# Performance work log

Hardware: AMD Instinct MI355X
Metric: run time of the kernel (lower is better)

The kernel has to match this reference:

```python
import jax, jax.numpy as jnp
import numpy as np

ENZ_DIM, CPD_DIM, OUT_DIM = 1280, 256, 512
B, L_ENZ, L_CPD = 32, 512, 128
SCALE = OUT_DIM ** 0.5


def _linear_params(key, d_in, d_out):
    k1, k2 = jax.random.split(key)
    lim = 1.0 / np.sqrt(d_in)
    W = jax.random.uniform(k1, (d_in, d_out), jnp.float32, -lim, lim)
    b = jax.random.uniform(k2, (d_out,), jnp.float32, -lim, lim)
    return W, b


def setup_inputs() -> dict:
    key = jax.random.key(0)
    ks = jax.random.split(key, 16)
    inp = {
        "enz_node_feature": jax.random.normal(ks[0], (B, L_ENZ, ENZ_DIM), jnp.float32),
        "substrate_node_feature": jax.random.normal(ks[1], (B, L_CPD, CPD_DIM), jnp.float32),
        "product_node_feature": jax.random.normal(ks[2], (B, L_CPD, CPD_DIM), jnp.float32),
        "enz_node_feature_mask": jnp.ones((B, L_ENZ), dtype=bool),
        "substrate_node_feature_mask": jnp.ones((B, L_CPD), dtype=bool),
        "product_node_feature_mask": jnp.ones((B, L_CPD), dtype=bool),
        "interaction_weight": jax.random.normal(ks[3], (B, L_CPD, L_ENZ), jnp.float32),
    }
    # cross_attn_enzyme: query=enz (ENZ_DIM), key/value=cpd (CPD_DIM)
    inp["enz_Wq"], inp["enz_bq"] = _linear_params(ks[4], ENZ_DIM, OUT_DIM)
    inp["enz_Wk"], inp["enz_bk"] = _linear_params(ks[5], CPD_DIM, OUT_DIM)
    inp["enz_Wv"], inp["enz_bv"] = _linear_params(ks[6], CPD_DIM, OUT_DIM)
    # cross_attn_substrate: query=cpd, key/value=enz
    inp["sub_Wq"], inp["sub_bq"] = _linear_params(ks[7], CPD_DIM, OUT_DIM)
    inp["sub_Wk"], inp["sub_bk"] = _linear_params(ks[8], ENZ_DIM, OUT_DIM)
    inp["sub_Wv"], inp["sub_bv"] = _linear_params(ks[9], ENZ_DIM, OUT_DIM)
    # cross_attn_product: query=cpd, key/value=enz
    inp["prod_Wq"], inp["prod_bq"] = _linear_params(ks[10], CPD_DIM, OUT_DIM)
    inp["prod_Wk"], inp["prod_bk"] = _linear_params(ks[11], ENZ_DIM, OUT_DIM)
    inp["prod_Wv"], inp["prod_bv"] = _linear_params(ks[12], ENZ_DIM, OUT_DIM)
    return inp


def _cross_attn(q_in, k_in, v_in, q_mask, k_mask, Wq, bq, Wk, bk, Wv, bv, attn_bias=None):
    q = q_in @ Wq + bq          # [B, Lq, D]
    k = k_in @ Wk + bk          # [B, Lk, D]
    v = v_in @ Wv + bv          # [B, Lk, D]
    scores = jnp.einsum("bqd,bkd->bqk", q, k) / SCALE
    if attn_bias is not None:
        scores = scores + attn_bias
    mask = q_mask[:, :, None] & k_mask[:, None, :]   # [B, Lq, Lk]
    scores = jnp.where(mask, scores, -1e9)
    w = jax.nn.softmax(scores, axis=-1)
    return jnp.einsum("bqk,bkd->bqd", w, v)


def reference(enz_node_feature, substrate_node_feature, product_node_feature,
              enz_node_feature_mask, substrate_node_feature_mask, product_node_feature_mask,
              interaction_weight,
              enz_Wq, enz_bq, enz_Wk, enz_bk, enz_Wv, enz_bv,
              sub_Wq, sub_bq, sub_Wk, sub_bk, sub_Wv, sub_bv,
              prod_Wq, prod_bq, prod_Wk, prod_bk, prod_Wv, prod_bv):
    subs_pocket_weight = interaction_weight                       # [B, L_cpd, L_enz]
    pocket_subs_weight = jnp.swapaxes(interaction_weight, 1, 2)   # [B, L_enz, L_cpd]

    enzyme_subs = _cross_attn(enz_node_feature, substrate_node_feature, substrate_node_feature,
                              enz_node_feature_mask, substrate_node_feature_mask,
                              enz_Wq, enz_bq, enz_Wk, enz_bk, enz_Wv, enz_bv,
                              attn_bias=pocket_subs_weight)
    subs_enzyme = _cross_attn(substrate_node_feature, enz_node_feature, enz_node_feature,
                              substrate_node_feature_mask, enz_node_feature_mask,
                              sub_Wq, sub_bq, sub_Wk, sub_bk, sub_Wv, sub_bv,
                              attn_bias=subs_pocket_weight)
    # product path reuses cross_attn_enzyme weights for enz->prod (as in torch code)
    enzyme_prod = _cross_attn(enz_node_feature, product_node_feature, product_node_feature,
                              enz_node_feature_mask, product_node_feature_mask,
                              enz_Wq, enz_bq, enz_Wk, enz_bk, enz_Wv, enz_bv)
    prod_enzyme = _cross_attn(product_node_feature, enz_node_feature, enz_node_feature,
                              product_node_feature_mask, enz_node_feature_mask,
                              prod_Wq, prod_bq, prod_Wk, prod_bk, prod_Wv, prod_bv)

    return jnp.concatenate([enzyme_subs.mean(axis=1), subs_enzyme.mean(axis=1),
                            enzyme_prod.mean(axis=1), prod_enzyme.mean(axis=1)], axis=-1)
```

## Files before the change

### kernel.cpp

```cpp
#include <hip/hip_runtime.h>
#include <cstdint>
#include <cstddef>


#define SCALE_INV 0.044194173824159216f

typedef short bf16x8 __attribute__((ext_vector_type(8)));
typedef float f32x4  __attribute__((ext_vector_type(4)));

__device__ __forceinline__ ushort f2bf(float f) {
  union { float f; unsigned u; } c; c.f = f;
  unsigned u = c.u + 0x7fffu + ((c.u >> 16) & 1u);
  return (ushort)(u >> 16);
}
__device__ __forceinline__ float bf2f(ushort h) {
  return __uint_as_float(((unsigned)h) << 16);
}
__device__ __forceinline__ void gload16(const ushort* g, ushort* l) {
  __builtin_amdgcn_global_load_lds(
      (const __attribute__((address_space(1))) void*)g,
      (__attribute__((address_space(3))) void*)l, 16, 0, 0);
}

__device__ __forceinline__ void cvt8(const float* __restrict__ in,
                                     ushort* __restrict__ out, int blk, int n) {
  int i = (blk * 256 + (int)threadIdx.x) * 8;
  if (i >= n) return;
  float4 a = *(const float4*)(in + i);
  float4 b = *(const float4*)(in + i + 4);
  ushort o[8] = { f2bf(a.x), f2bf(a.y), f2bf(a.z), f2bf(a.w),
                  f2bf(b.x), f2bf(b.y), f2bf(b.z), f2bf(b.w) };
  *(uint4*)(out + i) = *(uint4*)o;
}

__global__ __launch_bounds__(256) void prep_fused(
    const float* __restrict__ enz, const float* __restrict__ sub,
    const float* __restrict__ prod,
    ushort* __restrict__ enz_b, ushort* __restrict__ sub_b, ushort* __restrict__ prod_b,
    const float* __restrict__ enz_Wq, const float* __restrict__ enz_Wk,
    const float* __restrict__ sub_Wq, const float* __restrict__ sub_Wk,
    const float* __restrict__ prod_Wq, const float* __restrict__ prod_Wk,
    ushort* __restrict__ eWq_b, ushort* __restrict__ eWk_b,
    ushort* __restrict__ sWq_b, ushort* __restrict__ sWk_b,
    ushort* __restrict__ pWq_b, ushort* __restrict__ pWk_b,
    const float* __restrict__ enz_bq, const float* __restrict__ sub_bq,
    const float* __restrict__ prod_bq,
    const float* __restrict__ enz_bv, const float* __restrict__ sub_bv,
    const float* __restrict__ prod_bv,
    ushort* __restrict__ W3t, float* __restrict__ u_e_s,
    float* __restrict__ zero_base, float* __restrict__ out)
{
  const int f = blockIdx.x, t = threadIdx.x;
  if (f < 10240) { cvt8(enz, enz_b, f, 20971520); return; }
  if (f < 10752) { cvt8(sub, sub_b, f - 10240, 1048576); return; }
  if (f < 11264) { cvt8(prod, prod_b, f - 10752, 1048576); return; }
  if (f < 12416) {
    const int l = f - 11264;
    if (l < 320)       cvt8(enz_Wq,  eWq_b, l,        655360);
    else if (l < 640)  cvt8(sub_Wk,  sWk_b, l - 320,  655360);
    else if (l < 960)  cvt8(prod_Wk, pWk_b, l - 640,  655360);
    else if (l < 1024) cvt8(enz_Wk,  eWk_b, l - 960,  131072);
    else if (l < 1088) cvt8(sub_Wq,  sWq_b, l - 1024, 131072);
    else               cvt8(prod_Wq, pWq_b, l - 1088, 131072);
    return;
  }
  if (f < 12592) {
    const int g = f - 12416;
    const float* W; const float* bv; int d0, kind;
    if (g < 80)       { W = sub_Wk;  bv = sub_bq;  d0 = g * 16;         kind = 0; }
    else if (g < 160) { W = prod_Wk; bv = prod_bq; d0 = (g - 80) * 16;  kind = 1; }
    else              { W = enz_Wk;  bv = enz_bq;  d0 = (g - 160) * 16; kind = 2; }
    const int r = t >> 4, i = t & 15, d = d0 + r;
    const float* row = W + (size_t)d * 512;
    float s = 0.f;
#pragma unroll
    for (int j = 0; j < 32; j++) s += row[i + j * 16] * bv[i + j * 16];
    s += __shfl_xor(s, 1); s += __shfl_xor(s, 2);
    s += __shfl_xor(s, 4); s += __shfl_xor(s, 8);
    if (i == 0) {
      if (kind < 2) W3t[(size_t)(768 + kind) * 1280 + d] = f2bf(s);
      else          u_e_s[d] = s * SCALE_INV;
    }
    return;
  }
  if (f < 13168) { zero_base[(f - 12592) * 256 + t] = 0.f; return; }
  if (f < 13803) {
    const int idx = (f - 13168) * 256 + t;
    ((unsigned*)(W3t + (size_t)770 * 1280))[idx] = 0u;
    return;
  }
  {
    const int idx = (f - 13803) * 256 + t;
    const int col = idx & 2047;
    const int q = col >> 9, n = col & 511;
    const float* bvp = (q == 1) ? sub_bv : (q == 3) ? prod_bv : enz_bv;
    out[idx] = bvp[n];
  }
}

__device__ __forceinline__ void mfma_tile(
    const ushort* __restrict__ A, int lda,
    const ushort* __restrict__ Bt, int ldb, int K,
    int bm, int bn, ushort* AsBase, ushort* BsBase, f32x4 (&acc)[4][4])
{
  const int t = threadIdx.x, wave = t >> 6, lane = t & 63;
  const int srow = wave * 16 + (lane >> 2);
  const int sseg = (lane & 3) * 8;
  const ushort* Ag0 = A + (size_t)(bm + srow) * lda + sseg;
  const ushort* Ag1 = Ag0 + (size_t)64 * lda;
  const ushort* Bg0 = Bt + (size_t)(bn + srow) * ldb + sseg;
  const ushort* Bg1 = Bg0 + (size_t)64 * ldb;
  ushort* AsP0 = AsBase + srow * 32 + sseg;
  ushort* AsP1 = AsP0 + 64 * 32;
  ushort* BsP0 = BsBase + srow * 32 + sseg;
  ushort* BsP1 = BsP0 + 64 * 32;
  const int wm = (wave >> 1) * 64, wn = (wave & 1) * 64;
  const int fl = lane & 15, fq = lane >> 4;
  const bf16x8* ArP = (const bf16x8*)(AsBase + (wm + fl) * 32 + fq * 8);
  const bf16x8* BrP = (const bf16x8*)(BsBase + (wn + fl) * 32 + fq * 8);
  for (int k0 = 0; k0 < K; k0 += 32) {
    __syncthreads();
    gload16(Ag0 + k0, AsP0);
    gload16(Ag1 + k0, AsP1);
    gload16(Bg0 + k0, BsP0);
    gload16(Bg1 + k0, BsP1);
    __syncthreads();
    bf16x8 af[4], bfr[4];
#pragma unroll
    for (int i = 0; i < 4; i++) af[i] = ArP[i * 64];
#pragma unroll
    for (int j = 0; j < 4; j++) bfr[j] = BrP[j * 64];
#pragma unroll
    for (int i = 0; i < 4; i++)
#pragma unroll
      for (int j = 0; j < 4; j++)
        acc[i][j] = __builtin_amdgcn_mfma_f32_16x16x32_bf16(af[i], bfr[j], acc[i][j], 0, 0, 0);
  }
}

__global__ __launch_bounds__(256) void fold_w3(
    const ushort* __restrict__ eWq_b, const ushort* __restrict__ eWk_b,
    const ushort* __restrict__ sWq_b, const ushort* __restrict__ sWk_b,
    const ushort* __restrict__ pWq_b, const ushort* __restrict__ pWk_b,
    const ushort* __restrict__ sub_b, const ushort* __restrict__ prod_b,
    const float* __restrict__ u_e_s,
    ushort* __restrict__ W3t, float* __restrict__ t_es, float* __restrict__ t_ep)
{
  __shared__ __align__(16) ushort As[128 * 32];
  __shared__ __align__(16) ushort Bs[128 * 32];
  __shared__ float us[256];
  const int f = blockIdx.x, t = threadIdx.x;
  if (f >= 60) {
    const int g = f - 60, path = g >> 3, blk8 = g & 7;
    const ushort* Xb = path ? prod_b : sub_b;
    float* T = path ? t_ep : t_es;
    us[t] = u_e_s[t];
    __syncthreads();
#pragma unroll
    for (int e = 0; e < 2; ++e) {
      const int row = blk8 * 512 + e * 256 + t;
      const ushort* xr = Xb + (size_t)row * 256;
      float s = 0.f;
      for (int c = 0; c < 256; c += 8) {
        bf16x8 v = *(const bf16x8*)(xr + c);
#pragma unroll
        for (int i = 0; i < 8; ++i) s += bf2f((ushort)v[i]) * us[c + i];
      }
      T[row] = s;
    }
    return;
  }
  const int seg = f / 20, l = f % 20;
  const int bm = (l / 10) * 128, bn = (l % 10) * 128;
  const ushort* A  = (seg == 0) ? eWk_b : (seg == 1) ? sWq_b : pWq_b;
  const ushort* Bt = (seg == 0) ? eWq_b : (seg == 1) ? sWk_b : pWk_b;
  f32x4 acc[4][4] = {};
  mfma_tile(A, 512, Bt, 512, 512, bm, bn, As, Bs, acc);
  const int lane = t & 63, wave = t >> 6;
  const int wm = (wave >> 1) * 64, wn = (wave & 1) * 64;
  const int fl = lane & 15, fq = lane >> 4;
#pragma unroll
  for (int i = 0; i < 4; i++)
#pragma unroll
    for (int j = 0; j < 4; j++) {
      const int col = bn + wn + j * 16 + fl;
#pragma unroll
      for (int r = 0; r < 4; r++) {
        const int row = seg * 256 + bm + wm + i * 16 + fq * 4 + r;
        W3t[(size_t)row * 1280 + col] = f2bf(acc[i][j][r]);
      }
    }
}

__device__ __forceinline__ void yg_stage_half(
    const ushort* __restrict__ gbase, int k0, int h,
    ushort* ldsTile, int wv, int l, int srow8, int scol)
{
  const int row0 = h * 128 + wv * 16 + srow8;
  const ushort* g0 = gbase + (size_t)row0 * 1280 + k0 + scol;
  ushort* d0 = ldsTile + h * 8192 + wv * 1024 + l * 8;
  gload16(g0, d0);
  gload16(g0 + (size_t)8 * 1280, d0 + 512);
}

__device__ __forceinline__ bf16x8 yg_frag(const ushort* tile, int row, int kk, int fq) {
  const int X = (kk * 64 + fq * 16) ^ ((row & 7) << 4);
  return *(const bf16x8*)((const char*)tile + row * 128 + X);
}

__global__ __launch_bounds__(512, 2) void y_gemm(
    const ushort* __restrict__ A,
    const ushort* __restrict__ B,
    ushort* __restrict__ Y)
{
  extern __shared__ __align__(16) ushort lds[];
  const int t = threadIdx.x;
  const int wv = t >> 6, l = t & 63;
  const int fl = l & 15, fq = l >> 4;
  const int f = blockIdx.x;
  const int xcd = f & 7, slot = f >> 3;
  const int mt = xcd * 8 + (slot >> 2), nt = slot & 3;
  const int bm = mt * 256, bn = nt * 256;
  const int wm = (wv >> 2) * 128, wn = (wv & 3) * 64;
  const int nfr = (bn != 768) ? 4 : (((wv & 3) == 0) ? 1 : 0);
  const int srow8 = l >> 3;
  const int scol = 8 * ((l & 7) ^ srow8);
  const ushort* Ag = A + (size_t)bm * 1280;
  const ushort* Bg = B + (size_t)bn * 1280;

  f32x4 acc[8][4] = {};

  yg_stage_half(Ag, 0, 0, lds, wv, l, srow8, scol);
  yg_stage_half(Ag, 0, 1, lds, wv, l, srow8, scol);
  yg_stage_half(Bg, 0, 0, lds + 16384, wv, l, srow8, scol);
  yg_stage_half(Bg, 0, 1, lds + 16384, wv, l, srow8, scol);
  yg_stage_half(Ag, 64, 0, lds + 32768, wv, l, srow8, scol);
  yg_stage_half(Ag, 64, 1, lds + 32768, wv, l, srow8, scol);
  asm volatile("s_waitcnt vmcnt(4)" ::: "memory");
  __builtin_amdgcn_s_barrier();
  __builtin_amdgcn_sched_barrier(0);

  for (int j = 0; j < 20; ++j) {
    const int p = j & 1;
    const ushort* At = lds + p * 32768;
    const ushort* Bt = At + 16384;
    ushort* Ao = (ushort*)(lds + (p ^ 1) * 32768);
    ushort* Bo = Ao + 16384;
    const int kn = (j + 1) * 64;

    bf16x8 bf_[4][2];
    if (nfr > 0) {
#pragma unroll
      for (int n = 0; n < 4; ++n) if (n < nfr)
#pragma unroll
        for (int kk = 0; kk < 2; ++kk)
          bf_[n][kk] = yg_frag(Bt, wn + n * 16 + fl, kk, fq);
    }

#pragma unroll
    for (int mp = 0; mp < 4; ++mp) {
      if (mp == 0 && j < 19) yg_stage_half(Bg, kn, 0, Bo, wv, l, srow8, scol);
      if (mp == 1 && j < 19) yg_stage_half(Bg, kn, 1, Bo, wv, l, srow8, scol);
      if (nfr > 0) {
        bf16x8 a0[2], a1[2];
#pragma unroll
        for (int kk = 0; kk < 2; ++kk) {
          a0[kk] = yg_frag(At, wm + (mp * 2) * 16 + fl, kk, fq);
          a1[kk] = yg_frag(At, wm + (mp * 2 + 1) * 16 + fl, kk, fq);
        }
        __builtin_amdgcn_s_setprio(1);
#pragma unroll
        for (int kk = 0; kk < 2; ++kk)
#pragma unroll
          for (int n = 0; n < 4; ++n) if (n < nfr) {
            acc[mp * 2][n] = __builtin_amdgcn_mfma_f32_16x16x32_bf16(
                a0[kk], bf_[n][kk], acc[mp * 2][n], 0, 0, 0);
            acc[mp * 2 + 1][n] = __builtin_amdgcn_mfma_f32_16x16x32_bf16(
                a1[kk], bf_[n][kk], acc[mp * 2 + 1][n], 0, 0, 0);
          }
        __builtin_amdgcn_s_setprio(0);
      }
      if (mp < 3) __builtin_amdgcn_s_barrier();
    }

    asm volatile("" ::: "memory");
    __builtin_amdgcn_s_barrier();
    if (j + 2 < 20) {
      yg_stage_half(Ag, (j + 2) * 64, 0, (ushort*)At, wv, l, srow8, scol);
      yg_stage_half(Ag, (j + 2) * 64, 1, (ushort*)At, wv, l, srow8, scol);
    }
    if (j < 18) asm volatile("s_waitcnt vmcnt(4)" ::: "memory");
    else        asm volatile("s_waitcnt vmcnt(0)" ::: "memory");
    __builtin_amdgcn_s_barrier();
    __builtin_amdgcn_sched_barrier(0);
  }

#pragma unroll
  for (int m = 0; m < 8; ++m)
#pragma unroll
    for (int n = 0; n < 4; ++n) if (n < nfr) {
#pragma unroll
      for (int r = 0; r < 4; ++r) {
        const int row = bm + wm + m * 16 + fq * 4 + r;
        const int col = bn + wn + n * 16 + fl;
        Y[(size_t)row * 1024 + col] = f2bf(acc[m][n][r]);
      }
    }
}

__global__ __launch_bounds__(256) void score_fused(
    const ushort* __restrict__ Y, const ushort* __restrict__ sub_b,
    const ushort* __restrict__ prod_b, const float* __restrict__ iw,
    const float* __restrict__ t_es, const float* __restrict__ t_ep,
    float* __restrict__ Sc_se, float* __restrict__ Sc_pe,
    float* __restrict__ l_se, float* __restrict__ l_pe,
    float* __restrict__ wsum_es, float* __restrict__ wsum_ep)
{
  __shared__ __align__(16) ushort As[128 * 32];
  __shared__ __align__(16) ushort Bs[128 * 32];
  __shared__ float red[2][128];
  __shared__ float red2[2][128];
  const int f = blockIdx.x, t = threadIdx.x;
  const int lane = t & 63, wave = t >> 6;
  const int wm = (wave >> 1) * 64, wn = (wave & 1) * 64;
  const int fl = lane & 15, fq = lane >> 4;
  f32x4 acc[4][4] = {};

  if (f < 256) {
    const int path = f >> 7, l = f & 127, b = l & 31, mt = l >> 5;
    const int bm = mt * 128;
    const ushort* X = (path ? prod_b : sub_b) + (size_t)b * 32768;
    mfma_tile(Y + (size_t)b * 512 * 1024, 1024, X, 256, 256, bm, 0, As, Bs, acc);
    const size_t ib = (size_t)b * 65536;
    const float* Tp = (path ? t_ep : t_es) + b * 128;
    float tvv[4];
#pragma unroll
    for (int j = 0; j < 4; j++) tvv[j] = Tp[wn + j * 16 + fl];
    float rsum[4][4];
#pragma unroll
    for (int i = 0; i < 4; i++)
#pragma unroll
      for (int r = 0; r < 4; r++) rsum[i][r] = 0.f;
#pragma unroll
    for (int i = 0; i < 4; i++)
#pragma unroll
      for (int j = 0; j < 4; j++)
#pragma unroll
        for (int r = 0; r < 4; r++) {
          const int row = wm + i * 16 + fq * 4 + r;
          const int col = wn + j * 16 + fl;
          float s = acc[i][j][r] * SCALE_INV + tvv[j];
          if (path == 0) s += iw[ib + (size_t)col * 512 + (bm + row)];
          const float e = __expf(s);
          acc[i][j][r] = e;
          rsum[i][r] += e;
        }
#pragma unroll
    for (int m = 1; m <= 8; m <<= 1)
#pragma unroll
      for (int i = 0; i < 4; i++)
#pragma unroll
        for (int r = 0; r < 4; r++)
          rsum[i][r] += __shfl_xor(rsum[i][r], m);
    if (fl == 0)
#pragma unroll
      for (int i = 0; i < 4; i++)
#pragma unroll
        for (int r = 0; r < 4; r++)
          red[wave & 1][wm + i * 16 + fq * 4 + r] = rsum[i][r];
    __syncthreads();
    float csum[4] = { 0.f, 0.f, 0.f, 0.f };
#pragma unroll
    for (int i = 0; i < 4; i++)
#pragma unroll
      for (int r = 0; r < 4; r++) {
        const int row = wm + i * 16 + fq * 4 + r;
        const float invr = 1.f / (red[0][row] + red[1][row]);
#pragma unroll
        for (int j = 0; j < 4; j++) csum[j] += acc[i][j][r] * invr;
      }
#pragma unroll
    for (int m = 16; m <= 32; m <<= 1)
#pragma unroll
      for (int j = 0; j < 4; j++) csum[j] += __shfl_xor(csum[j], m);
    if (fq == 0)
#pragma unroll
      for (int j = 0; j < 4; j++) red2[wave >> 1][wn + j * 16 + fl] = csum[j];
    __syncthreads();
    float* ws = (path ? wsum_ep : wsum_es) + b * 128;
    if (t < 128) atomicAdd(&ws[t], red2[0][t] + red2[1][t]);
  } else {
    const int g = f - 256, path = g >> 7, l = g & 127, b = l & 31, nt = l >> 5;
    const int bn = nt * 128;
    const ushort* A  = (path ? prod_b : sub_b) + (size_t)b * 32768;
    const ushort* Bt = Y + (size_t)b * 512 * 1024 + 256 + path * 256;
    mfma_tile(A, 256, Bt, 1024, 256, 0, bn, As, Bs, acc);
    const size_t ib = (size_t)b * 65536;
    float* Sc = (path ? Sc_pe : Sc_se) + ib;
    float tv[4];
#pragma unroll
    for (int j = 0; j < 4; j++) {
      const int col = wn + j * 16 + fl;
      tv[j] = bf2f(Y[(size_t)(b * 512 + bn + col) * 1024 + 768 + path]) * SCALE_INV;
    }
    float rsum[4][4];
#pragma unroll
    for (int i = 0; i < 4; i++)
#pragma unroll
      for (int r = 0; r < 4; r++) rsum[i][r] = 0.f;
#pragma unroll
    for (int i = 0; i < 4; i++)
#pragma unroll
      for (int j = 0; j < 4; j++)
#pragma unroll
        for (int r = 0; r < 4; r++) {
          const int row = wm + i * 16 + fq * 4 + r;
          const int col = wn + j * 16 + fl;
          float s = acc[i][j][r] * SCALE_INV + tv[j];
          if (path == 0) s += iw[ib + (size_t)row * 512 + (bn + col)];
          const float e = __expf(s);
          Sc[(size_t)row * 512 + bn + col] = e;
          rsum[i][r] += e;
        }
#pragma unroll
    for (int m = 1; m <= 8; m <<= 1)
#pragma unroll
      for (int i = 0; i < 4; i++)
#pragma unroll
        for (int r = 0; r < 4; r++)
          rsum[i][r] += __shfl_xor(rsum[i][r], m);
    if (fl == 0)
#pragma unroll
      for (int i = 0; i < 4; i++)
#pragma unroll
        for (int r = 0; r < 4; r++)
          red[wave & 1][wm + i * 16 + fq * 4 + r] = rsum[i][r];
    __syncthreads();
    float* lr = (path ? l_pe : l_se) + b * 128;
    if (t < 128) atomicAdd(&lr[t], red[0][t] + red[1][t]);
  }
}

__global__ __launch_bounds__(256) void colsum2(
    const float* __restrict__ Sc_se, const float* __restrict__ Sc_pe,
    const float* __restrict__ l_se, const float* __restrict__ l_pe,
    float* __restrict__ wsum_se, float* __restrict__ wsum_pe)
{
  __shared__ float inv[32];
  const int f = blockIdx.x, t = threadIdx.x;
  const int path = f >> 7, l = f & 127, b = l & 31, qc = l >> 5;
  const float* Sc = (path ? Sc_pe : Sc_se) + (size_t)b * 65536 + (size_t)(qc * 32) * 512;
  const float* lv = (path ? l_pe : l_se) + b * 128 + qc * 32;
  float* ws = (path ? wsum_pe : wsum_se) + b * 512;
  if (t < 32) inv[t] = 1.f / lv[t];
  __syncthreads();
  float a0 = 0.f, a1 = 0.f;
  for (int q = 0; q < 32; q++) {
    const float iq = inv[q];
    a0 += Sc[(size_t)q * 512 + t] * iq;
    a1 += Sc[(size_t)q * 512 + 256 + t] * iq;
  }
  atomicAdd(&ws[t], a0);
  atomicAdd(&ws[t + 256], a1);
}

__global__ __launch_bounds__(256) void wx_fused(
    const float* __restrict__ wsum_se, const float* __restrict__ wsum_pe,
    const float* __restrict__ wsum_es, const float* __restrict__ wsum_ep,
    const ushort* __restrict__ enz_b, const ushort* __restrict__ sub_b,
    const ushort* __restrict__ prod_b,
    float* __restrict__ wx_se, float* __restrict__ wx_pe,
    float* __restrict__ wx_es, float* __restrict__ wx_ep)
{
  __shared__ float wse[256], wpe[256];
  const int f = blockIdx.x, t = threadIdx.x;
  if (f < 320) {
    const int ch = f % 5, tmp = f / 5, b = tmp & 31, kh = tmp >> 5;
    wse[t] = wsum_se[b * 512 + kh * 256 + t];
    wpe[t] = wsum_pe[b * 512 + kh * 256 + t];
    __syncthreads();
    const int c = ch * 256 + t;
    const ushort* X = enz_b + (size_t)b * 512 * 1280 + (size_t)(kh * 256) * 1280 + c;
    float a_se = 0.f, a_pe = 0.f;
#pragma unroll 4
    for (int k = 0; k < 256; k++) {
      const float x = bf2f(X[(size_t)k * 1280]);
      a_se += wse[k] * x;
      a_pe += wpe[k] * x;
    }
    atomicAdd(&wx_se[b * 1280 + c], a_se);
    atomicAdd(&wx_pe[b * 1280 + c], a_pe);
  } else if (f < 352) {
    const int b = f - 320;
    const ushort* X = sub_b + (size_t)b * 128 * 256 + t;
    float a = 0.f;
#pragma unroll 4
    for (int k = 0; k < 128; k++) a += wsum_es[b * 128 + k] * bf2f(X[(size_t)k * 256]);
    wx_es[b * 256 + t] = a;
  } else {
    const int b = f - 352;
    const ushort* X = prod_b + (size_t)b * 128 * 256 + t;
    float a = 0.f;
#pragma unroll 4
    for (int k = 0; k < 128; k++) a += wsum_ep[b * 128 + k] * bf2f(X[(size_t)k * 256]);
    wx_ep[b * 256 + t] = a;
  }
}

__global__ __launch_bounds__(256) void out_gemv(
    const float* __restrict__ wx_es, const float* __restrict__ wx_se,
    const float* __restrict__ wx_ep, const float* __restrict__ wx_pe,
    const float* __restrict__ enz_Wv, const float* __restrict__ sub_Wv,
    const float* __restrict__ prod_Wv,
    float* __restrict__ out)
{
  __shared__ float sw[32][64];
  const int f = blockIdx.x, t = threadIdx.x;
  const float* wx; const float* Wv; int Cdim, qoff, nb, cc; float inv;
  if (f < 40)      { wx = wx_se; Wv = sub_Wv;  Cdim = 1280; inv = 1.f / 128.f; qoff = 512;  nb = f & 1;        cc = f >> 1; }
  else if (f < 80) { wx = wx_pe; Wv = prod_Wv; Cdim = 1280; inv = 1.f / 128.f; qoff = 1536; nb = (f - 40) & 1; cc = (f - 40) >> 1; }
  else if (f < 88) { wx = wx_es; Wv = enz_Wv;  Cdim = 256;  inv = 1.f / 512.f; qoff = 0;    nb = (f - 80) & 1; cc = (f - 80) >> 1; }
  else             { wx = wx_ep; Wv = enz_Wv;  Cdim = 256;  inv = 1.f / 512.f; qoff = 1024; nb = (f - 88) & 1; cc = (f - 88) >> 1; }
  const int c0 = cc * 64, n = nb * 256 + t;
#pragma unroll
  for (int i = 0; i < 8; i++) {
    const int idx = t + i * 256, b = idx >> 6, c = idx & 63;
    sw[b][c] = wx[(size_t)b * Cdim + c0 + c];
  }
  __syncthreads();
  float acc[32];
#pragma unroll
  for (int b = 0; b < 32; b++) acc[b] = 0.f;
  for (int c = 0; c < 64; c += 4) {
    const float w0 = Wv[(size_t)(c0 + c) * 512 + n];
    const float w1 = Wv[(size_t)(c0 + c + 1) * 512 + n];
    const float w2 = Wv[(size_t)(c0 + c + 2) * 512 + n];
    const float w3 = Wv[(size_t)(c0 + c + 3) * 512 + n];
#pragma unroll
    for (int b = 0; b < 32; b++) {
      const float4 s = *(const float4*)&sw[b][c];
      acc[b] += s.x * w0 + s.y * w1 + s.z * w2 + s.w * w3;
    }
  }
#pragma unroll
  for (int b = 0; b < 32; b++)
    atomicAdd(&out[(size_t)b * 2048 + qoff + n], acc[b] * inv);
}

extern "C" void kernel_launch(void* const* d_in, const int* in_sizes, int n_in,
                              void* d_out, int out_size, void* d_ws, size_t ws_size,
                              hipStream_t stream)
{
  (void)in_sizes; (void)n_in; (void)out_size; (void)ws_size;
  const float* enz     = (const float*)d_in[0];
  const float* sub     = (const float*)d_in[1];
  const float* prod    = (const float*)d_in[2];
  const float* iw      = (const float*)d_in[6];
  const float* enz_Wq  = (const float*)d_in[7];
  const float* enz_bq  = (const float*)d_in[8];
  const float* enz_Wk  = (const float*)d_in[9];
  const float* enz_Wv  = (const float*)d_in[11];
  const float* enz_bv  = (const float*)d_in[12];
  const float* sub_Wq  = (const float*)d_in[13];
  const float* sub_bq  = (const float*)d_in[14];
  const float* sub_Wk  = (const float*)d_in[15];
  const float* sub_Wv  = (const float*)d_in[17];
  const float* sub_bv  = (const float*)d_in[18];
  const float* prod_Wq = (const float*)d_in[19];
  const float* prod_bq = (const float*)d_in[20];
  const float* prod_Wk = (const float*)d_in[21];
  const float* prod_Wv = (const float*)d_in[23];
  const float* prod_bv = (const float*)d_in[24];
  float* out = (float*)d_out;

  char* wsb = (char*)d_ws;
  size_t off = 0;
  auto alloc = [&](size_t bytes) {
    void* p = wsb + off;
    off += (bytes + 255) & ~(size_t)255;
    return p;
  };
  ushort* enz_b   = (ushort*)alloc((size_t)32 * 512 * 1280 * 2);
  ushort* sub_b   = (ushort*)alloc((size_t)32 * 128 * 256 * 2);
  ushort* prod_b  = (ushort*)alloc((size_t)32 * 128 * 256 * 2);
  ushort* eWq_b   = (ushort*)alloc((size_t)1280 * 512 * 2);
  ushort* sWk_b   = (ushort*)alloc((size_t)1280 * 512 * 2);
  ushort* pWk_b   = (ushort*)alloc((size_t)1280 * 512 * 2);
  ushort* eWk_b   = (ushort*)alloc((size_t)256 * 512 * 2);
  ushort* sWq_b   = (ushort*)alloc((size_t)256 * 512 * 2);
  ushort* pWq_b   = (ushort*)alloc((size_t)256 * 512 * 2);
  ushort* W3t     = (ushort*)alloc((size_t)1024 * 1280 * 2);
  ushort* Y       = (ushort*)alloc((size_t)16384 * 1024 * 2);
  float*  u_e_s   = (float*)alloc(256 * 4);
  float*  t_es    = (float*)alloc(4096 * 4);
  float*  t_ep    = (float*)alloc(4096 * 4);
  float*  Sc_se   = (float*)alloc((size_t)32 * 128 * 512 * 4);
  float*  Sc_pe   = (float*)alloc((size_t)32 * 128 * 512 * 4);
  float* wsum_es = (float*)alloc(4096 * 4);
  float* wsum_ep = (float*)alloc(4096 * 4);
  float* wsum_se = (float*)alloc(16384 * 4);
  float* wsum_pe = (float*)alloc(16384 * 4);
  float* l_se    = (float*)alloc(4096 * 4);
  float* l_pe    = (float*)alloc(4096 * 4);
  float* wx_se   = (float*)alloc(40960 * 4);
  float* wx_pe   = (float*)alloc(40960 * 4);
  float* wx_es   = (float*)alloc(8192 * 4);
  float* wx_ep   = (float*)alloc(8192 * 4);

  static bool ygemm_attr_set = false;
  if (!ygemm_attr_set) {
    hipFuncSetAttribute(reinterpret_cast<const void*>(y_gemm),
                        hipFuncAttributeMaxDynamicSharedMemorySize, 131072);
    ygemm_attr_set = true;
  }

  const dim3 blk(256);

  prep_fused<<<14059, blk, 0, stream>>>(
      enz, sub, prod, enz_b, sub_b, prod_b,
      enz_Wq, enz_Wk, sub_Wq, sub_Wk, prod_Wq, prod_Wk,
      eWq_b, eWk_b, sWq_b, sWk_b, pWq_b, pWk_b,
      enz_bq, sub_bq, prod_bq, enz_bv, sub_bv, prod_bv,
      W3t, u_e_s, wsum_es, out);

  fold_w3<<<76, blk, 0, stream>>>(
      eWq_b, eWk_b, sWq_b, sWk_b, pWq_b, pWk_b,
      sub_b, prod_b, u_e_s, W3t, t_es, t_ep);

  y_gemm<<<256, 512, 131072, stream>>>(enz_b, W3t, Y);

  score_fused<<<512, blk, 0, stream>>>(
      Y, sub_b, prod_b, iw, t_es, t_ep, Sc_se, Sc_pe, l_se, l_pe,
      wsum_es, wsum_ep);

  colsum2<<<256, blk, 0, stream>>>(Sc_se, Sc_pe, l_se, l_pe, wsum_se, wsum_pe);

  wx_fused<<<384, blk, 0, stream>>>(
      wsum_se, wsum_pe, wsum_es, wsum_ep, enz_b, sub_b, prod_b,
      wx_se, wx_pe, wx_es, wx_ep);

  out_gemv<<<96, blk, 0, stream>>>(
      wx_es, wx_se, wx_ep, wx_pe, enz_Wv, sub_Wv, prod_Wv, out);
}
```

Measured before the change: 318.4 us.

## Shrink Y GEMM to 768 columns and compute bias-term dot products separately

The two extra bias columns (enz·Wk·bq for sub and prod paths) were packed into a 1024-wide W3t, so the Y GEMM ran a mostly empty fourth column tile of 256. They are now computed as separate GEMVs over enz_b in extra fold_w3 blocks, and the Y GEMM tile changes from 256x256 to 256x192, covering exactly 768 columns with no idle waves. LDS staging is restructured into 64-row units with separate A/B double buffers, and intermediate barriers inside the mp loop are removed. The cost is an extra pass reading enz_b (about 40MB in bf16) in fold_w3, plus the risk of LDS races now that those barriers are gone.

```diff
diff --git a/kernel.cpp b/kernel.cpp
--- a/kernel.cpp
+++ b/kernel.cpp
@@ -47,7 +47,8 @@
     const float* __restrict__ prod_bq,
     const float* __restrict__ enz_bv, const float* __restrict__ sub_bv,
     const float* __restrict__ prod_bv,
-    ushort* __restrict__ W3t, float* __restrict__ u_e_s,
+    float* __restrict__ u_s_s, float* __restrict__ u_p_s,
+    float* __restrict__ u_e_s,
     float* __restrict__ zero_base, float* __restrict__ out)
 {
   const int f = blockIdx.x, t = threadIdx.x;
@@ -66,10 +67,10 @@
   }
   if (f < 12592) {
     const int g = f - 12416;
-    const float* W; const float* bv; int d0, kind;
-    if (g < 80)       { W = sub_Wk;  bv = sub_bq;  d0 = g * 16;         kind = 0; }
-    else if (g < 160) { W = prod_Wk; bv = prod_bq; d0 = (g - 80) * 16;  kind = 1; }
-    else              { W = enz_Wk;  bv = enz_bq;  d0 = (g - 160) * 16; kind = 2; }
+    const float* W; const float* bv; float* U; int d0;
+    if (g < 80)       { W = sub_Wk;  bv = sub_bq;  U = u_s_s; d0 = g * 16; }
+    else if (g < 160) { W = prod_Wk; bv = prod_bq; U = u_p_s; d0 = (g - 80) * 16; }
+    else              { W = enz_Wk;  bv = enz_bq;  U = u_e_s; d0 = (g - 160) * 16; }
     const int r = t >> 4, i = t & 15, d = d0 + r;
     const float* row = W + (size_t)d * 512;
     float s = 0.f;
@@ -77,20 +78,12 @@
     for (int j = 0; j < 32; j++) s += row[i + j * 16] * bv[i + j * 16];
     s += __shfl_xor(s, 1); s += __shfl_xor(s, 2);
     s += __shfl_xor(s, 4); s += __shfl_xor(s, 8);
-    if (i == 0) {
-      if (kind < 2) W3t[(size_t)(768 + kind) * 1280 + d] = f2bf(s);
-      else          u_e_s[d] = s * SCALE_INV;
-    }
+    if (i == 0) U[d] = s * SCALE_INV;
     return;
   }
   if (f < 13168) { zero_base[(f - 12592) * 256 + t] = 0.f; return; }
-  if (f < 13803) {
+  {
     const int idx = (f - 13168) * 256 + t;
-    ((unsigned*)(W3t + (size_t)770 * 1280))[idx] = 0u;
-    return;
-  }
-  {
-    const int idx = (f - 13803) * 256 + t;
     const int col = idx & 2047;
     const int q = col >> 9, n = col & 511;
     const float* bvp = (q == 1) ? sub_bv : (q == 3) ? prod_bv : enz_bv;
@@ -143,13 +136,45 @@
     const ushort* __restrict__ sWq_b, const ushort* __restrict__ sWk_b,
     const ushort* __restrict__ pWq_b, const ushort* __restrict__ pWk_b,
     const ushort* __restrict__ sub_b, const ushort* __restrict__ prod_b,
-    const float* __restrict__ u_e_s,
-    ushort* __restrict__ W3t, float* __restrict__ t_es, float* __restrict__ t_ep)
+    const ushort* __restrict__ enz_b,
+    const float* __restrict__ u_e_s, const float* __restrict__ u_s_s,
+    const float* __restrict__ u_p_s,
+    ushort* __restrict__ W3t, float* __restrict__ t_es, float* __restrict__ t_ep,
+    float* __restrict__ t_se, float* __restrict__ t_pe)
 {
   __shared__ __align__(16) ushort As[128 * 32];
   __shared__ __align__(16) ushort Bs[128 * 32];
   __shared__ float us[256];
+  __shared__ float us2[2][1280];
   const int f = blockIdx.x, t = threadIdx.x;
+  if (f >= 76) {
+    const int g2 = f - 76;
+    for (int i = t; i < 1280; i += 256) { us2[0][i] = u_s_s[i]; us2[1][i] = u_p_s[i]; }
+    __syncthreads();
+    const int lane16 = t & 15, rg = t >> 4;
+    for (int p = 0; p < 16; ++p) {
+      const int row = g2 * 256 + p * 16 + rg;
+      const ushort* xr = enz_b + (size_t)row * 1280;
+      float ss = 0.f, sp = 0.f;
+#pragma unroll
+      for (int q = 0; q < 10; ++q) {
+        const int c0 = q * 128 + lane16 * 8;
+        bf16x8 v = *(const bf16x8*)(xr + c0);
+#pragma unroll
+        for (int i = 0; i < 8; ++i) {
+          const float x = bf2f((ushort)v[i]);
+          ss += x * us2[0][c0 + i];
+          sp += x * us2[1][c0 + i];
+        }
+      }
+      ss += __shfl_xor(ss, 1); ss += __shfl_xor(ss, 2);
+      ss += __shfl_xor(ss, 4); ss += __shfl_xor(ss, 8);
+      sp += __shfl_xor(sp, 1); sp += __shfl_xor(sp, 2);
+      sp += __shfl_xor(sp, 4); sp += __shfl_xor(sp, 8);
+      if (lane16 == 0) { t_se[row] = ss; t_pe[row] = sp; }
+    }
+    return;
+  }
   if (f >= 60) {
     const int g = f - 60, path = g >> 3, blk8 = g & 7;
     const ushort* Xb = path ? prod_b : sub_b;
@@ -192,15 +217,13 @@
     }
 }
 
-__device__ __forceinline__ void yg_stage_half(
-    const ushort* __restrict__ gbase, int k0, int h,
+__device__ __forceinline__ void yg_stage_unit(
+    const ushort* __restrict__ gbase, int k0, int u,
     ushort* ldsTile, int wv, int l, int srow8, int scol)
 {
-  const int row0 = h * 128 + wv * 16 + srow8;
-  const ushort* g0 = gbase + (size_t)row0 * 1280 + k0 + scol;
-  ushort* d0 = ldsTile + h * 8192 + wv * 1024 + l * 8;
-  gload16(g0, d0);
-  gload16(g0 + (size_t)8 * 1280, d0 + 512);
+  const int row0 = u * 64 + wv * 8 + srow8;
+  gload16(gbase + (size_t)row0 * 1280 + k0 + scol,
+          ldsTile + u * 4096 + wv * 512 + l * 8);
 }
 
 __device__ __forceinline__ bf16x8 yg_frag(const ushort* tile, int row, int kk, int fq) {
@@ -220,74 +243,73 @@
   const int f = blockIdx.x;
   const int xcd = f & 7, slot = f >> 3;
   const int mt = xcd * 8 + (slot >> 2), nt = slot & 3;
-  const int bm = mt * 256, bn = nt * 256;
-  const int wm = (wv >> 2) * 128, wn = (wv & 3) * 64;
-  const int nfr = (bn != 768) ? 4 : (((wv & 3) == 0) ? 1 : 0);
+  const int bm = mt * 256, bn = nt * 192;
+  const int wm = (wv >> 2) * 128, wn = (wv & 3) * 48;
   const int srow8 = l >> 3;
   const int scol = 8 * ((l & 7) ^ srow8);
   const ushort* Ag = A + (size_t)bm * 1280;
   const ushort* Bg = B + (size_t)bn * 1280;
 
-  f32x4 acc[8][4] = {};
-
-  yg_stage_half(Ag, 0, 0, lds, wv, l, srow8, scol);
-  yg_stage_half(Ag, 0, 1, lds, wv, l, srow8, scol);
-  yg_stage_half(Bg, 0, 0, lds + 16384, wv, l, srow8, scol);
-  yg_stage_half(Bg, 0, 1, lds + 16384, wv, l, srow8, scol);
-  yg_stage_half(Ag, 64, 0, lds + 32768, wv, l, srow8, scol);
-  yg_stage_half(Ag, 64, 1, lds + 32768, wv, l, srow8, scol);
+  ushort* A0 = lds;
+  ushort* B0 = lds + 16384;
+  ushort* A1 = lds + 28672;
+  ushort* B1 = lds + 45056;
+
+  f32x4 acc[8][3] = {};
+
+#pragma unroll
+  for (int u = 0; u < 4; ++u) yg_stage_unit(Ag, 0, u, A0, wv, l, srow8, scol);
+#pragma unroll
+  for (int u = 0; u < 3; ++u) yg_stage_unit(Bg, 0, u, B0, wv, l, srow8, scol);
+#pragma unroll
+  for (int u = 0; u < 4; ++u) yg_stage_unit(Ag, 64, u, A1, wv, l, srow8, scol);
   asm volatile("s_waitcnt vmcnt(4)" ::: "memory");
   __builtin_amdgcn_s_barrier();
   __builtin_amdgcn_sched_barrier(0);
 
   for (int j = 0; j < 20; ++j) {
     const int p = j & 1;
-    const ushort* At = lds + p * 32768;
-    const ushort* Bt = At + 16384;
-    ushort* Ao = (ushort*)(lds + (p ^ 1) * 32768);
-    ushort* Bo = Ao + 16384;
+    const ushort* At = p ? A1 : A0;
+    const ushort* Bt = p ? B1 : B0;
+    ushort* Bo = p ? B0 : B1;
     const int kn = (j + 1) * 64;
 
-    bf16x8 bf_[4][2];
-    if (nfr > 0) {
-#pragma unroll
-      for (int n = 0; n < 4; ++n) if (n < nfr)
-#pragma unroll
-        for (int kk = 0; kk < 2; ++kk)
-          bf_[n][kk] = yg_frag(Bt, wn + n * 16 + fl, kk, fq);
-    }
+    bf16x8 bf_[3][2];
+#pragma unroll
+    for (int n = 0; n < 3; ++n)
+#pragma unroll
+      for (int kk = 0; kk < 2; ++kk)
+        bf_[n][kk] = yg_frag(Bt, wn + n * 16 + fl, kk, fq);
 
 #pragma unroll
     for (int mp = 0; mp < 4; ++mp) {
-      if (mp == 0 && j < 19) yg_stage_half(Bg, kn, 0, Bo, wv, l, srow8, scol);
-      if (mp == 1 && j < 19) yg_stage_half(Bg, kn, 1, Bo, wv, l, srow8, scol);
-      if (nfr > 0) {
-        bf16x8 a0[2], a1[2];
-#pragma unroll
-        for (int kk = 0; kk < 2; ++kk) {
-          a0[kk] = yg_frag(At, wm + (mp * 2) * 16 + fl, kk, fq);
-          a1[kk] = yg_frag(At, wm + (mp * 2 + 1) * 16 + fl, kk, fq);
+      if (mp < 3 && j < 19) yg_stage_unit(Bg, kn, mp, Bo, wv, l, srow8, scol);
+      bf16x8 a0[2], a1v[2];
+#pragma unroll
+      for (int kk = 0; kk < 2; ++kk) {
+        a0[kk]  = yg_frag(At, wm + (mp * 2) * 16 + fl, kk, fq);
+        a1v[kk] = yg_frag(At, wm + (mp * 2 + 1) * 16 + fl, kk, fq);
+      }
+      __builtin_amdgcn_s_setprio(1);
+#pragma unroll
+      for (int kk = 0; kk < 2; ++kk)
+#pragma unroll
+        for (int n = 0; n < 3; ++n) {
+          acc[mp * 2][n] = __builtin_amdgcn_mfma_f32_16x16x32_bf16(
+              a0[kk], bf_[n][kk], acc[mp * 2][n], 0, 0, 0);
+          acc[mp * 2 + 1][n] = __builtin_amdgcn_mfma_f32_16x16x32_bf16(
+              a1v[kk], bf_[n][kk], acc[mp * 2 + 1][n], 0, 0, 0);
         }
-        __builtin_amdgcn_s_setprio(1);
-#pragma unroll
-        for (int kk = 0; kk < 2; ++kk)
-#pragma unroll
-          for (int n = 0; n < 4; ++n) if (n < nfr) {
-            acc[mp * 2][n] = __builtin_amdgcn_mfma_f32_16x16x32_bf16(
-                a0[kk], bf_[n][kk], acc[mp * 2][n], 0, 0, 0);
-            acc[mp * 2 + 1][n] = __builtin_amdgcn_mfma_f32_16x16x32_bf16(
-                a1[kk], bf_[n][kk], acc[mp * 2 + 1][n], 0, 0, 0);
-          }
-        __builtin_amdgcn_s_setprio(0);
-      }
-      if (mp < 3) __builtin_amdgcn_s_barrier();
+      __builtin_amdgcn_s_setprio(0);
     }
 
     asm volatile("" ::: "memory");
     __builtin_amdgcn_s_barrier();
     if (j + 2 < 20) {
-      yg_stage_half(Ag, (j + 2) * 64, 0, (ushort*)At, wv, l, srow8, scol);
-      yg_stage_half(Ag, (j + 2) * 64, 1, (ushort*)At, wv, l, srow8, scol);
+      ushort* Ao = (ushort*)At;
+#pragma unroll
+      for (int u = 0; u < 4; ++u)
+        yg_stage_unit(Ag, (j + 2) * 64, u, Ao, wv, l, srow8, scol);
     }
     if (j < 18) asm volatile("s_waitcnt vmcnt(4)" ::: "memory");
     else        asm volatile("s_waitcnt vmcnt(0)" ::: "memory");
@@ -298,20 +320,20 @@
 #pragma unroll
   for (int m = 0; m < 8; ++m)
 #pragma unroll
-    for (int n = 0; n < 4; ++n) if (n < nfr) {
+    for (int n = 0; n < 3; ++n)
 #pragma unroll
       for (int r = 0; r < 4; ++r) {
         const int row = bm + wm + m * 16 + fq * 4 + r;
         const int col = bn + wn + n * 16 + fl;
-        Y[(size_t)row * 1024 + col] = f2bf(acc[m][n][r]);
+        Y[(size_t)row * 768 + col] = f2bf(acc[m][n][r]);
       }
-    }
 }
 
 __global__ __launch_bounds__(256) void score_fused(
     const ushort* __restrict__ Y, const ushort* __restrict__ sub_b,
     const ushort* __restrict__ prod_b, const float* __restrict__ iw,
     const float* __restrict__ t_es, const float* __restrict__ t_ep,
+    const float* __restrict__ t_se, const float* __restrict__ t_pe,
     float* __restrict__ Sc_se, float* __restrict__ Sc_pe,
     float* __restrict__ l_se, float* __restrict__ l_pe,
     float* __restrict__ wsum_es, float* __restrict__ wsum_ep)
@@ -330,7 +352,7 @@
     const int path = f >> 7, l = f & 127, b = l & 31, mt = l >> 5;
     const int bm = mt * 128;
     const ushort* X = (path ? prod_b : sub_b) + (size_t)b * 32768;
-    mfma_tile(Y + (size_t)b * 512 * 1024, 1024, X, 256, 256, bm, 0, As, Bs, acc);
+    mfma_tile(Y + (size_t)b * 512 * 768, 768, X, 256, 256, bm, 0, As, Bs, acc);
     const size_t ib = (size_t)b * 65536;
     const float* Tp = (path ? t_ep : t_es) + b * 128;
     float tvv[4];
@@ -393,16 +415,14 @@
     const int g = f - 256, path = g >> 7, l = g & 127, b = l & 31, nt = l >> 5;
     const int bn = nt * 128;
     const ushort* A  = (path ? prod_b : sub_b) + (size_t)b * 32768;
-    const ushort* Bt = Y + (size_t)b * 512 * 1024 + 256 + path * 256;
-    mfma_tile(A, 256, Bt, 1024, 256, 0, bn, As, Bs, acc);
+    const ushort* Bt = Y + (size_t)b * 512 * 768 + 256 + path * 256;
+    mfma_tile(A, 256, Bt, 768, 256, 0, bn, As, Bs, acc);
     const size_t ib = (size_t)b * 65536;
     float* Sc = (path ? Sc_pe : Sc_se) + ib;
+    const float* Tq = (path ? t_pe : t_se) + b * 512;
     float tv[4];
 #pragma unroll
-    for (int j = 0; j < 4; j++) {
-      const int col = wn + j * 16 + fl;
-      tv[j] = bf2f(Y[(size_t)(b * 512 + bn + col) * 1024 + 768 + path]) * SCALE_INV;
-    }
+    for (int j = 0; j < 4; j++) tv[j] = Tq[bn + wn + j * 16 + fl];
     float rsum[4][4];
 #pragma unroll
     for (int i = 0; i < 4; i++)
@@ -589,11 +609,15 @@
   ushort* eWk_b   = (ushort*)alloc((size_t)256 * 512 * 2);
   ushort* sWq_b   = (ushort*)alloc((size_t)256 * 512 * 2);
   ushort* pWq_b   = (ushort*)alloc((size_t)256 * 512 * 2);
-  ushort* W3t     = (ushort*)alloc((size_t)1024 * 1280 * 2);
-  ushort* Y       = (ushort*)alloc((size_t)16384 * 1024 * 2);
+  ushort* W3t     = (ushort*)alloc((size_t)768 * 1280 * 2);
+  ushort* Y       = (ushort*)alloc((size_t)16384 * 768 * 2);
+  float*  u_s_s   = (float*)alloc(1280 * 4);
+  float*  u_p_s   = (float*)alloc(1280 * 4);
   float*  u_e_s   = (float*)alloc(256 * 4);
   float*  t_es    = (float*)alloc(4096 * 4);
   float*  t_ep    = (float*)alloc(4096 * 4);
+  float*  t_se    = (float*)alloc(16384 * 4);
+  float*  t_pe    = (float*)alloc(16384 * 4);
   float*  Sc_se   = (float*)alloc((size_t)32 * 128 * 512 * 4);
   float*  Sc_pe   = (float*)alloc((size_t)32 * 128 * 512 * 4);
   float* wsum_es = (float*)alloc(4096 * 4);
@@ -610,28 +634,29 @@
   static bool ygemm_attr_set = false;
   if (!ygemm_attr_set) {
     hipFuncSetAttribute(reinterpret_cast<const void*>(y_gemm),
-                        hipFuncAttributeMaxDynamicSharedMemorySize, 131072);
+                        hipFuncAttributeMaxDynamicSharedMemorySize, 114688);
     ygemm_attr_set = true;
   }
 
   const dim3 blk(256);
 
-  prep_fused<<<14059, blk, 0, stream>>>(
+  prep_fused<<<13424, blk, 0, stream>>>(
       enz, sub, prod, enz_b, sub_b, prod_b,
       enz_Wq, enz_Wk, sub_Wq, sub_Wk, prod_Wq, prod_Wk,
       eWq_b, eWk_b, sWq_b, sWk_b, pWq_b, pWk_b,
       enz_bq, sub_bq, prod_bq, enz_bv, sub_bv, prod_bv,
-      W3t, u_e_s, wsum_es, out);
-
-  fold_w3<<<76, blk, 0, stream>>>(
+      u_s_s, u_p_s, u_e_s, wsum_es, out);
+
+  fold_w3<<<140, blk, 0, stream>>>(
       eWq_b, eWk_b, sWq_b, sWk_b, pWq_b, pWk_b,
-      sub_b, prod_b, u_e_s, W3t, t_es, t_ep);
-
-  y_gemm<<<256, 512, 131072, stream>>>(enz_b, W3t, Y);
+      sub_b, prod_b, enz_b, u_e_s, u_s_s, u_p_s,
+      W3t, t_es, t_ep, t_se, t_pe);
+
+  y_gemm<<<256, 512, 114688, stream>>>(enz_b, W3t, Y);
 
   score_fused<<<512, blk, 0, stream>>>(
-      Y, sub_b, prod_b, iw, t_es, t_ep, Sc_se, Sc_pe, l_se, l_pe,
-      wsum_es, wsum_ep);
+      Y, sub_b, prod_b, iw, t_es, t_ep, t_se, t_pe,
+      Sc_se, Sc_pe, l_se, l_pe, wsum_es, wsum_ep);
 
   colsum2<<<256, blk, 0, stream>>>(Sc_se, Sc_pe, l_se, l_pe, wsum_se, wsum_pe);
 
```

Result: no change. 313.3 us (median of 2 runs) (-1.6%).
